# Kernel tuning notes

Hardware: AMD Instinct MI355X
Metric: run time of the kernel (lower is better)

## Reference

```python
import jax, jax.numpy as jnp
import numpy as np

T, B, N_IN, N_OUT = 100, 32, 1024, 512
LR_LTP, LR_LTD = 1e-4, -1e-4
TAU_PRE, TAU_POST, DT = 20.0, 20.0, 1.0
W_MIN, W_MAX = 0.0, 1.0
SPIKE_PROB = 0.05


def setup_inputs() -> dict:
    key = jax.random.key(0)
    k1, k2, k3 = jax.random.split(key, 3)
    weight = jax.random.uniform(k1, (N_OUT, N_IN), dtype=jnp.float32)
    pre_spikes = (jax.random.uniform(k2, (T, B, N_IN)) < SPIKE_PROB).astype(jnp.float32)
    post_spikes = (jax.random.uniform(k3, (T, B, N_OUT)) < SPIKE_PROB).astype(jnp.float32)
    pre_trace = jnp.zeros((B, N_IN), jnp.float32)
    post_trace = jnp.zeros((B, N_OUT), jnp.float32)
    return {"weight": weight, "pre_spikes": pre_spikes, "post_spikes": post_spikes,
            "pre_trace": pre_trace, "post_trace": post_trace}


def reference(weight, pre_spikes, post_spikes, pre_trace, post_trace):
    # weight: [N_out, N_in]; pre_spikes: [T,B,N_in]; post_spikes: [T,B,N_out]
    decay_pre = jnp.exp(jnp.asarray(-DT / TAU_PRE, weight.dtype))
    decay_post = jnp.exp(jnp.asarray(-DT / TAU_POST, weight.dtype))
    # Soft bounds (w_max=1.0 > 0 -> w_max - w; w_min=0.0 not < 0 -> w)
    soft_ltp = W_MAX - weight
    soft_ltd = weight
    Bf = jnp.asarray(pre_spikes.shape[1], weight.dtype)

    def step(carry, xs):
        pre_tr, post_tr, dw = carry
        pre_s, post_s = xs  # [B,N_in], [B,N_out]
        pre_tr = pre_tr * decay_pre + pre_s
        post_tr = post_tr * decay_post + post_s
        # batch-mean of outer products -> [N_out, N_in]
        ltp_mean = jnp.einsum('bo,bi->oi', post_s, pre_tr) / Bf
        ltd_mean = jnp.einsum('bo,bi->oi', post_tr, pre_s) / Bf
        dw = dw + LR_LTP * soft_ltp * ltp_mean + LR_LTD * soft_ltd * ltd_mean
        return (pre_tr, post_tr, dw), None

    init = (pre_trace, post_trace, jnp.zeros_like(weight))
    (pre_tr, post_tr, delta_w), _ = jax.lax.scan(step, init, (pre_spikes, post_spikes))
    return delta_w, pre_tr, post_tr
```

## Files before the change

### kernel.cpp

```cpp
#include <hip/hip_runtime.h>

typedef unsigned short ushort;
typedef unsigned int uint;
typedef unsigned char uchar;
typedef __attribute__((ext_vector_type(8))) int intx8;
typedef __attribute__((ext_vector_type(16))) float floatx16;

#define T_STEPS 100
#define BATCH   32
#define NIN     1024
#define NOUT    512

#define SEG      128
#define KPAD     (BATCH * SEG)
#define KSTRIDEB 4160
#define KS       16
#define KCHUNK   (KPAD / KS)

#define LR_LTP  (1e-4f)
#define LR_LTD  (-1e-4f)
#define INV_B   (1.0f / 32.0f)
#define DECAY   0.951229424500714f
#define D32     0.201896517994655f
#define TCH     32
#define NCHUNK  4

#define OFF_PRE  (NOUT * NIN)
#define OFF_POST (OFF_PRE + BATCH * NIN)

#define B_PRST  0
#define B_PRTT  ((size_t)NIN * KSTRIDEB)
#define B_POST  ((size_t)2 * NIN * KSTRIDEB)
#define B_POTT  ((size_t)2 * NIN * KSTRIDEB + (size_t)NOUT * KSTRIDEB)
#define B_END   ((size_t)2 * (NIN + NOUT) * KSTRIDEB)
#define SLABU   (NOUT * NIN + 128)


static __device__ __forceinline__ uint pk4_fp8(float a, float b, float c, float d) {
    uint v = 0;
    v = __builtin_amdgcn_cvt_pk_fp8_f32(a, b, v, false);
    v = __builtin_amdgcn_cvt_pk_fp8_f32(c, d, v, true);
    return v;
}

static __device__ __forceinline__ ushort f2bf(float f) {
    union { float f; unsigned int u; } v; v.f = f;
    unsigned int r = (v.u + 0x7FFFu + ((v.u >> 16) & 1u)) >> 16;
    return (ushort)r;
}

__global__ __launch_bounds__(256) void stdp_traces_t(
    const float* __restrict__ pre_s,
    const float* __restrict__ post_s,
    const float* __restrict__ pre_tr0,
    const float* __restrict__ post_tr0,
    uchar* __restrict__ pre_s_t, uchar* __restrict__ pre_tr_t,
    uchar* __restrict__ post_s_t, uchar* __restrict__ post_tr_t,
    float* __restrict__ out)
{
    __shared__ uint Ls[64 * 33];
    __shared__ uint Lt[64 * 33];
    __shared__ float Eend[NCHUNK][64];

    const int chain = threadIdx.x & 63;
    const int c     = threadIdx.x >> 6;
    const int g     = blockIdx.x * 64 + chain;

    const float* src; const float* init;
    int id, stride, outoff;
    if (g < BATCH * NIN) {
        src = pre_s;  init = pre_tr0;
        id = g;               stride = BATCH * NIN;  outoff = OFF_PRE;
    } else {
        src = post_s; init = post_tr0;
        id = g - BATCH * NIN; stride = BATCH * NOUT; outoff = OFF_POST;
    }

    const int t0 = c * TCH;
    float x[TCH];
    #pragma unroll
    for (int m = 0; m < TCH; ++m)
        x[m] = (t0 + m < T_STEPS) ? src[(size_t)(t0 + m) * stride + id] : 0.f;

    uint sp[8];
    #pragma unroll
    for (int j = 0; j < 8; ++j)
        sp[j] = pk4_fp8(x[4*j], x[4*j+1], x[4*j+2], x[4*j+3]);

    float e = 0.f;
    #pragma unroll
    for (int m = 0; m < TCH; ++m) { e = e * DECAY + x[m]; x[m] = e; }
    Eend[c][chain] = e;
    __syncthreads();

    float C = init[id];
    for (int cc = 0; cc < c; ++cc) C = C * D32 + Eend[cc][chain];
    float p = C * DECAY;
    #pragma unroll
    for (int m = 0; m < TCH; ++m) { x[m] += p; p *= DECAY; }

    if (c == NCHUNK - 1) out[outoff + id] = x[3];

    #pragma unroll
    for (int j = 0; j < 8; ++j) {
        const uint tj = pk4_fp8(x[4*j], x[4*j+1], x[4*j+2], x[4*j+3]);
        Ls[chain * 33 + c * 8 + j] = sp[j];
        Lt[chain * 33 + c * 8 + j] = tj;
    }
    __syncthreads();

    const int id0 = blockIdx.x * 64;
    uchar *dS, *dT; int b0, ch0;
    if (id0 < BATCH * NIN) {
        b0 = id0 >> 10; ch0 = id0 & 1023; dS = pre_s_t;  dT = pre_tr_t;
    } else {
        const int idq = id0 - BATCH * NIN;
        b0 = idq >> 9;  ch0 = idq & 511;  dS = post_s_t; dT = post_tr_t;
    }
    #pragma unroll
    for (int j = 0; j < 4; ++j) {
        const int q  = threadIdx.x + 256 * j;
        const int op = q >> 9;
        const int qq = q & 511;
        const int r  = qq >> 3;
        const int cc = qq & 7;
        const uint* l = (op ? Lt : Ls) + r * 33 + cc * 4;
        const uint4 v = make_uint4(l[0], l[1], l[2], l[3]);
        uchar* gd = (op ? dT : dS) + (size_t)(ch0 + r) * KSTRIDEB + b0 * SEG + cc * 16;
        *(uint4*)gd = v;
    }
}

static __device__ __forceinline__ intx8 ld32(const uchar* p) {
    const uint4 lo = *(const uint4*)p;
    const uint4 hv = *(const uint4*)(p + 16);
    intx8 r;
    r[0] = (int)lo.x; r[1] = (int)lo.y; r[2] = (int)lo.z; r[3] = (int)lo.w;
    r[4] = (int)hv.x; r[5] = (int)hv.y; r[6] = (int)hv.z; r[7] = (int)hv.w;
    return r;
}

__global__ __launch_bounds__(256, 2) void stdp_gemm_dual(
    const uchar* __restrict__ post_s_t, const uchar* __restrict__ pre_tr_t,
    const uchar* __restrict__ post_tr_t, const uchar* __restrict__ pre_s_t,
    const float* __restrict__ wmat, ushort* __restrict__ Spart)
{
    const int i0 = blockIdx.x * 128;
    const int o0 = blockIdx.y * 128;
    const int k0 = blockIdx.z * KCHUNK;

    const int tid  = threadIdx.x;
    const int w    = tid >> 6;
    const int lane = tid & 63;
    const int wm   = w & 1;
    const int wn   = w >> 1;
    const int l32  = lane & 31;
    const int hi   = lane >> 5;

    floatx16 accP[2][2], accD[2][2];
    #pragma unroll
    for (int mt = 0; mt < 2; ++mt)
        #pragma unroll
        for (int nt = 0; nt < 2; ++nt)
            #pragma unroll
            for (int r = 0; r < 16; ++r) {
                accP[mt][nt][r] = 0.f; accD[mt][nt][r] = 0.f;
            }

    const size_t aBase = (size_t)(o0 + wm * 64 + l32) * KSTRIDEB;
    const size_t bBase = (size_t)(i0 + wn * 64 + l32) * KSTRIDEB;

    for (int kb = k0; kb < k0 + KCHUNK; kb += 64) {
        const int ko = kb + (hi << 5);
        intx8 aP[2], aD[2], bP[2], bD[2];
        #pragma unroll
        for (int mt = 0; mt < 2; ++mt) {
            const size_t off = aBase + (size_t)(mt * 32) * KSTRIDEB + ko;
            aP[mt] = ld32(post_s_t  + off);
            aD[mt] = ld32(post_tr_t + off);
        }
        #pragma unroll
        for (int nt = 0; nt < 2; ++nt) {
            const size_t off = bBase + (size_t)(nt * 32) * KSTRIDEB + ko;
            bP[nt] = ld32(pre_tr_t + off);
            bD[nt] = ld32(pre_s_t  + off);
        }
        #pragma unroll
        for (int mt = 0; mt < 2; ++mt)
            #pragma unroll
            for (int nt = 0; nt < 2; ++nt) {
                accP[mt][nt] = __builtin_amdgcn_mfma_scale_f32_32x32x64_f8f6f4(
                    aP[mt], bP[nt], accP[mt][nt], 0, 0, 0, 127, 0, 127);
                accD[mt][nt] = __builtin_amdgcn_mfma_scale_f32_32x32x64_f8f6f4(
                    aD[mt], bD[nt], accD[mt][nt], 0, 0, 0, 127, 0, 127);
            }
    }

    ushort* Sz = Spart + (size_t)blockIdx.z * SLABU;
    const float c1 = LR_LTP * INV_B;
    const float c2 = LR_LTD * INV_B;
    #pragma unroll
    for (int mt = 0; mt < 2; ++mt) {
        const int ob = o0 + wm * 64 + mt * 32 + hi * 4;
        #pragma unroll
        for (int nt = 0; nt < 2; ++nt) {
            const int i = i0 + wn * 64 + nt * 32 + l32;
            #pragma unroll
            for (int r = 0; r < 16; ++r) {
                const int o = ob + (r & 3) + 8 * (r >> 2);
                const size_t idx = (size_t)o * NIN + i;
                const float wv = wmat[idx];
                const float v = c1 * (1.0f - wv) * accP[mt][nt][r]
                              + c2 * wv          * accD[mt][nt][r];
                Sz[idx] = f2bf(v);
            }
        }
    }
}

__global__ __launch_bounds__(128) void stdp_finalize(
    const ushort* __restrict__ Spart, float* __restrict__ out)
{
    const int j = blockIdx.x * blockDim.x + threadIdx.x;
    float s[8] = {0.f, 0.f, 0.f, 0.f, 0.f, 0.f, 0.f, 0.f};
    #pragma unroll
    for (int z = 0; z < KS; ++z) {
        const uint4 v = *(const uint4*)(Spart + (size_t)z * SLABU + (size_t)j * 8);
        const uint u[4] = {v.x, v.y, v.z, v.w};
        #pragma unroll
        for (int q = 0; q < 4; ++q) {
            union { uint u; float f; } lo, hi;
            lo.u = u[q] << 16;
            hi.u = u[q] & 0xFFFF0000u;
            s[2 * q]     += lo.f;
            s[2 * q + 1] += hi.f;
        }
    }
    float4* o = (float4*)(out + (size_t)j * 8);
    o[0] = make_float4(s[0], s[1], s[2], s[3]);
    o[1] = make_float4(s[4], s[5], s[6], s[7]);
}

extern "C" void kernel_launch(void* const* d_in, const int* in_sizes, int n_in,
                              void* d_out, int out_size, void* d_ws, size_t ws_size,
                              hipStream_t stream) {
    const float* weight   = (const float*)d_in[0];
    const float* pre_s    = (const float*)d_in[1];
    const float* post_s   = (const float*)d_in[2];
    const float* pre_tr0  = (const float*)d_in[3];
    const float* post_tr0 = (const float*)d_in[4];
    float* out = (float*)d_out;

    uchar* wsb = (uchar*)d_ws;
    uchar* pre_s_t   = wsb + B_PRST;
    uchar* pre_tr_t  = wsb + B_PRTT;
    uchar* post_s_t  = wsb + B_POST;
    uchar* post_tr_t = wsb + B_POTT;
    ushort* Spart    = (ushort*)(wsb + B_END);

    stdp_traces_t<<<dim3(BATCH * (NIN + NOUT) / 64), dim3(256), 0, stream>>>(
        pre_s, post_s, pre_tr0, post_tr0,
        pre_s_t, pre_tr_t, post_s_t, post_tr_t, out);

    stdp_gemm_dual<<<dim3(NIN / 128, NOUT / 128, KS), dim3(256), 0, stream>>>(
        post_s_t, pre_tr_t, post_tr_t, pre_s_t, weight, Spart);

    stdp_finalize<<<dim3((NOUT * NIN / 8) / 128), dim3(128), 0, stream>>>(
        Spart, out);
}
```

Measured before the change: 100.5 us.

## Shrink time padding to 112 per batch, halve split-K, narrow GEMM N-tile

Time chunks shrink from 32 to 28 steps, so each batch segment pads 100 steps to 112 instead of 128 and the GEMM K dimension drops. Split-K goes from 16 to 8 slabs, which cuts partial-sum traffic in the finalize pass. The N tile is halved to 64 so block count stays up, and the grid is reordered so the K-split index varies fastest, improving L2 reuse of the weight tile. The cost is lower per-block operand reuse (each A load now feeds fewer MFMAs) and a trace kernel with less regular indexing.

Result: faster. 98.41 us (median of 2 runs) (-2.1%).

```diff
diff --git a/kernel.cpp b/kernel.cpp
--- a/kernel.cpp
+++ b/kernel.cpp
@@ -11,18 +11,18 @@
 #define NIN     1024
 #define NOUT    512
 
-#define SEG      128
+#define SEG      112
 #define KPAD     (BATCH * SEG)
-#define KSTRIDEB 4160
-#define KS       16
+#define KSTRIDEB 3648
+#define KS       8
 #define KCHUNK   (KPAD / KS)
 
 #define LR_LTP  (1e-4f)
 #define LR_LTD  (-1e-4f)
 #define INV_B   (1.0f / 32.0f)
 #define DECAY   0.951229424500714f
-#define D32     0.201896517994655f
-#define TCH     32
+#define D28     0.246596963941607f
+#define TCH     28
 #define NCHUNK  4
 
 #define OFF_PRE  (NOUT * NIN)
@@ -82,9 +82,9 @@
     for (int m = 0; m < TCH; ++m)
         x[m] = (t0 + m < T_STEPS) ? src[(size_t)(t0 + m) * stride + id] : 0.f;
 
-    uint sp[8];
-    #pragma unroll
-    for (int j = 0; j < 8; ++j)
+    uint sp[7];
+    #pragma unroll
+    for (int j = 0; j < 7; ++j)
         sp[j] = pk4_fp8(x[4*j], x[4*j+1], x[4*j+2], x[4*j+3]);
 
     float e = 0.f;
@@ -94,18 +94,18 @@
     __syncthreads();
 
     float C = init[id];
-    for (int cc = 0; cc < c; ++cc) C = C * D32 + Eend[cc][chain];
+    for (int cc = 0; cc < c; ++cc) C = C * D28 + Eend[cc][chain];
     float p = C * DECAY;
     #pragma unroll
     for (int m = 0; m < TCH; ++m) { x[m] += p; p *= DECAY; }
 
-    if (c == NCHUNK - 1) out[outoff + id] = x[3];
-
-    #pragma unroll
-    for (int j = 0; j < 8; ++j) {
+    if (c == NCHUNK - 1) out[outoff + id] = x[15];
+
+    #pragma unroll
+    for (int j = 0; j < 7; ++j) {
         const uint tj = pk4_fp8(x[4*j], x[4*j+1], x[4*j+2], x[4*j+3]);
-        Ls[chain * 33 + c * 8 + j] = sp[j];
-        Lt[chain * 33 + c * 8 + j] = tj;
+        Ls[chain * 33 + c * 7 + j] = sp[j];
+        Lt[chain * 33 + c * 7 + j] = tj;
     }
     __syncthreads();
 
@@ -119,15 +119,17 @@
     }
     #pragma unroll
     for (int j = 0; j < 4; ++j) {
-        const int q  = threadIdx.x + 256 * j;
-        const int op = q >> 9;
-        const int qq = q & 511;
-        const int r  = qq >> 3;
-        const int cc = qq & 7;
-        const uint* l = (op ? Lt : Ls) + r * 33 + cc * 4;
-        const uint4 v = make_uint4(l[0], l[1], l[2], l[3]);
-        uchar* gd = (op ? dT : dS) + (size_t)(ch0 + r) * KSTRIDEB + b0 * SEG + cc * 16;
-        *(uint4*)gd = v;
+        const int q = threadIdx.x + 256 * j;
+        if (q < 896) {
+            const int op = q >= 448;
+            const int qq = q - op * 448;
+            const int r  = qq / 7;
+            const int cc = qq - r * 7;
+            const uint* l = (op ? Lt : Ls) + r * 33 + cc * 4;
+            const uint4 v = make_uint4(l[0], l[1], l[2], l[3]);
+            uchar* gd = (op ? dT : dS) + (size_t)(ch0 + r) * KSTRIDEB + b0 * SEG + cc * 16;
+            *(uint4*)gd = v;
+        }
     }
 }
 
@@ -145,9 +147,10 @@
     const uchar* __restrict__ post_tr_t, const uchar* __restrict__ pre_s_t,
     const float* __restrict__ wmat, ushort* __restrict__ Spart)
 {
-    const int i0 = blockIdx.x * 128;
-    const int o0 = blockIdx.y * 128;
-    const int k0 = blockIdx.z * KCHUNK;
+    const int kz = blockIdx.x;
+    const int i0 = blockIdx.y * 64;
+    const int o0 = blockIdx.z * 128;
+    const int k0 = kz * KCHUNK;
 
     const int tid  = threadIdx.x;
     const int w    = tid >> 6;
@@ -157,63 +160,53 @@
     const int l32  = lane & 31;
     const int hi   = lane >> 5;
 
-    floatx16 accP[2][2], accD[2][2];
+    floatx16 accP[2], accD[2];
     #pragma unroll
     for (int mt = 0; mt < 2; ++mt)
         #pragma unroll
-        for (int nt = 0; nt < 2; ++nt)
-            #pragma unroll
-            for (int r = 0; r < 16; ++r) {
-                accP[mt][nt][r] = 0.f; accD[mt][nt][r] = 0.f;
-            }
+        for (int r = 0; r < 16; ++r) { accP[mt][r] = 0.f; accD[mt][r] = 0.f; }
 
     const size_t aBase = (size_t)(o0 + wm * 64 + l32) * KSTRIDEB;
-    const size_t bBase = (size_t)(i0 + wn * 64 + l32) * KSTRIDEB;
+    const size_t bBase = (size_t)(i0 + wn * 32 + l32) * KSTRIDEB;
 
     for (int kb = k0; kb < k0 + KCHUNK; kb += 64) {
         const int ko = kb + (hi << 5);
-        intx8 aP[2], aD[2], bP[2], bD[2];
+        intx8 aP[2], aD[2], bP, bD;
         #pragma unroll
         for (int mt = 0; mt < 2; ++mt) {
             const size_t off = aBase + (size_t)(mt * 32) * KSTRIDEB + ko;
             aP[mt] = ld32(post_s_t  + off);
             aD[mt] = ld32(post_tr_t + off);
         }
-        #pragma unroll
-        for (int nt = 0; nt < 2; ++nt) {
-            const size_t off = bBase + (size_t)(nt * 32) * KSTRIDEB + ko;
-            bP[nt] = ld32(pre_tr_t + off);
-            bD[nt] = ld32(pre_s_t  + off);
-        }
-        #pragma unroll
-        for (int mt = 0; mt < 2; ++mt)
-            #pragma unroll
-            for (int nt = 0; nt < 2; ++nt) {
-                accP[mt][nt] = __builtin_amdgcn_mfma_scale_f32_32x32x64_f8f6f4(
-                    aP[mt], bP[nt], accP[mt][nt], 0, 0, 0, 127, 0, 127);
-                accD[mt][nt] = __builtin_amdgcn_mfma_scale_f32_32x32x64_f8f6f4(
-                    aD[mt], bD[nt], accD[mt][nt], 0, 0, 0, 127, 0, 127);
-            }
-    }
-
-    ushort* Sz = Spart + (size_t)blockIdx.z * SLABU;
+        {
+            const size_t off = bBase + ko;
+            bP = ld32(pre_tr_t + off);
+            bD = ld32(pre_s_t  + off);
+        }
+        #pragma unroll
+        for (int mt = 0; mt < 2; ++mt) {
+            accP[mt] = __builtin_amdgcn_mfma_scale_f32_32x32x64_f8f6f4(
+                aP[mt], bP, accP[mt], 0, 0, 0, 127, 0, 127);
+            accD[mt] = __builtin_amdgcn_mfma_scale_f32_32x32x64_f8f6f4(
+                aD[mt], bD, accD[mt], 0, 0, 0, 127, 0, 127);
+        }
+    }
+
+    ushort* Sz = Spart + (size_t)kz * SLABU;
     const float c1 = LR_LTP * INV_B;
     const float c2 = LR_LTD * INV_B;
     #pragma unroll
     for (int mt = 0; mt < 2; ++mt) {
         const int ob = o0 + wm * 64 + mt * 32 + hi * 4;
-        #pragma unroll
-        for (int nt = 0; nt < 2; ++nt) {
-            const int i = i0 + wn * 64 + nt * 32 + l32;
-            #pragma unroll
-            for (int r = 0; r < 16; ++r) {
-                const int o = ob + (r & 3) + 8 * (r >> 2);
-                const size_t idx = (size_t)o * NIN + i;
-                const float wv = wmat[idx];
-                const float v = c1 * (1.0f - wv) * accP[mt][nt][r]
-                              + c2 * wv          * accD[mt][nt][r];
-                Sz[idx] = f2bf(v);
-            }
+        const int i  = i0 + wn * 32 + l32;
+        #pragma unroll
+        for (int r = 0; r < 16; ++r) {
+            const int o = ob + (r & 3) + 8 * (r >> 2);
+            const size_t idx = (size_t)o * NIN + i;
+            const float wv = wmat[idx];
+            const float v = c1 * (1.0f - wv) * accP[mt][r]
+                          + c2 * wv          * accD[mt][r];
+            Sz[idx] = f2bf(v);
         }
     }
 }
@@ -262,7 +255,7 @@
         pre_s, post_s, pre_tr0, post_tr0,
         pre_s_t, pre_tr_t, post_s_t, post_tr_t, out);
 
-    stdp_gemm_dual<<<dim3(NIN / 128, NOUT / 128, KS), dim3(256), 0, stream>>>(
+    stdp_gemm_dual<<<dim3(KS, NIN / 64, NOUT / 128), dim3(256), 0, stream>>>(
         post_s_t, pre_tr_t, post_tr_t, pre_s_t, weight, Spart);
 
     stdp_finalize<<<dim3((NOUT * NIN / 8) / 128), dim3(128), 0, stream>>>(
```
